# Optimization experiments

Measured on AMD Instinct MI355X. Metric: run time of the kernel, lower is better.

Reference implementation:

```python
import jax, jax.numpy as jnp
import numpy as np

B, N, NC = 16, 25200, 80          # batch, raw predictions, classes (COCO)
CONF_THRES = 0.25
IOU_THRES = 0.45
MAX_CAND = 1000                    # candidates kept after score top-k (pre-NMS)
CLS_OFFSET = 4096.0                # class-wise box offset (non-agnostic NMS trick)
EPS = 1e-7


def setup_inputs() -> dict:
    key = jax.random.key(0)
    # raw head output: [x, y, w, h, obj, cls0..cls79], values in [0,1]
    pred = jax.random.uniform(key, (B, N, 5 + NC), dtype=jnp.float32)
    return {"pred": pred}


def _xywh2xyxy(x):
    xy, wh = x[..., :2], x[..., 2:4]
    return jnp.concatenate([xy - wh * 0.5, xy + wh * 0.5], axis=-1)


def _box_iou(boxes):
    # boxes: [C, 4] xyxy -> pairwise IoU [C, C]
    area = (boxes[:, 2] - boxes[:, 0]) * (boxes[:, 3] - boxes[:, 1])
    lt = jnp.maximum(boxes[:, None, :2], boxes[None, :, :2])
    rb = jnp.minimum(boxes[:, None, 2:], boxes[None, :, 2:])
    wh = jnp.clip(rb - lt, 0.0)
    inter = wh[..., 0] * wh[..., 1]
    return inter / (area[:, None] + area[None, :] - inter + EPS)


def _nms_single(p):
    # p: [N, 5+NC] -> (out [MAX_CAND, 6] xyxy/conf/cls zero-padded, keep [MAX_CAND] bool)
    obj = p[:, 4]
    cls_scores = p[:, 5:] * obj[:, None]          # conf = obj * cls
    conf = jnp.max(cls_scores, axis=-1)
    cls_idx = jnp.argmax(cls_scores, axis=-1)
    valid = (obj > CONF_THRES) & (conf > CONF_THRES)
    score = jnp.where(valid, conf, -1.0)

    # pre-NMS top-k by score (sorted descending) — fixed-shape stand-in for boolean filter
    top_scores, idx = jax.lax.top_k(score, MAX_CAND)
    boxes = _xywh2xyxy(p[idx, :4])                # [C, 4]
    kconf = conf[idx]
    kcls = cls_idx[idx].astype(jnp.float32)
    valid_c = top_scores > 0.0

    # class-offset boxes so different classes never overlap (agnostic=False)
    off_boxes = boxes + kcls[:, None] * CLS_OFFSET
    iou = _box_iou(off_boxes)                     # [C, C]

    ar = jnp.arange(MAX_CAND)

    def body(i, keep):
        sup = keep[i] & (iou[i] > IOU_THRES) & (ar > i)
        return keep & jnp.logical_not(sup)

    keep = jax.lax.fori_loop(0, MAX_CAND, body, valid_c)

    out = jnp.concatenate([boxes, kconf[:, None], kcls[:, None]], axis=-1)  # [C, 6]
    out = jnp.where(keep[:, None], out, 0.0)
    return out, keep


def reference(pred):
    out, keep = jax.vmap(_nms_single)(pred)
    return out, keep
```

## Files before the change

kernel.cpp:

```cpp
#include <hip/hip_runtime.h>
#include <stdint.h>

typedef unsigned int u32;
typedef unsigned long long u64;

#define BATCH 16
#define NANCH 25200
#define NCLS 80
#define ROWF 85
#define MAXC 1000
#define CONF_T 0.25f
#define IOU_T 0.45f
#define EPS_F 1e-7f
#define TILE 64
#define NTILES ((NANCH + TILE - 1) / TILE)

__device__ __forceinline__ float iou_ref(float4 a, float4 b) {
#pragma clang fp contract(off)
  float ai = (a.z - a.x) * (a.w - a.y);
  float aj = (b.z - b.x) * (b.w - b.y);
  float ltx = fmaxf(a.x, b.x), lty = fmaxf(a.y, b.y);
  float rbx = fminf(a.z, b.z), rby = fminf(a.w, b.w);
  float wx = fmaxf(rbx - ltx, 0.0f), wy = fmaxf(rby - lty, 0.0f);
  float inter = wx * wy;
  return inter / (ai + aj - inter + EPS_F);
}

__global__ __launch_bounds__(256) void k1_score(const float* __restrict__ pred,
                                                u64* __restrict__ keys,
                                                u32* __restrict__ hist) {
  __shared__ float srow[TILE * ROWF];
  __shared__ u64 skeys[TILE];
  __shared__ u32 lh[256];
  int tid = threadIdx.x;
  int b = blockIdx.y;
  int t0 = blockIdx.x * TILE;
  int ntile = (t0 + TILE <= NANCH) ? TILE : (NANCH - t0);
  int nf4 = (ntile * ROWF) >> 2;

  lh[tid] = 0;
  const float4* src4 = (const float4*)(pred + ((size_t)b * NANCH + t0) * ROWF);
  float4* smem4 = (float4*)srow;
#pragma unroll
  for (int k = 0; k < 6; ++k) {
    int i = k * 256 + tid;
    if (i < nf4) smem4[i] = src4[i];
  }
  __syncthreads();

  int a = tid >> 2;
  int q = tid & 3;
  float best = -1e30f;
  int bidx = 0;
  float obj = 0.0f;
  if (a < ntile) {
    const float* row = srow + a * ROWF;
    obj = row[4];
    int c0 = q * 20;
#pragma unroll
    for (int c = 0; c < 20; ++c) {
      float s = row[5 + c0 + c] * obj;
      if (s > best) { best = s; bidx = c0 + c; }
    }
  }
#pragma unroll
  for (int off = 1; off < 4; off <<= 1) {
    float ob = __shfl_xor(best, off);
    int oi = __shfl_xor(bidx, off);
    if (ob > best || (ob == best && oi < bidx)) { best = ob; bidx = oi; }
  }
  if (q == 0 && a < ntile) {
    int n = t0 + a;
    bool valid = (obj > CONF_T) && (best > CONF_T);
    u32 hi;
    if (valid) hi = __float_as_uint(best) | 0x80000000u;
    else hi = ((u32)n * 2654435761u) >> 1;
    u32 lo = ((u32)(32767 - n) << 7) | (u32)bidx;
    skeys[a] = ((u64)hi << 32) | lo;
    atomicAdd(&lh[hi >> 24], 1u);
  }
  __syncthreads();
  if (tid < ntile) keys[(size_t)b * NANCH + t0 + tid] = skeys[tid];
  u32 v = lh[tid];
  if (v) atomicAdd(&hist[b * 256 + tid], v);
}

__global__ __launch_bounds__(1024) void k2_select(const float* __restrict__ pred,
                                                  const u64* __restrict__ keys,
                                                  const u32* __restrict__ hist,
                                                  float* __restrict__ selbox,
                                                  float* __restrict__ offbox,
                                                  float* __restrict__ selconf,
                                                  float* __restrict__ selcls,
                                                  u32* __restrict__ selvalid) {
  int b = blockIdx.x;
  int tid = threadIdx.x;
  __shared__ u32 h[256];
  __shared__ u32 sh_sel;
  __shared__ int sh_rank;
  __shared__ u32 scount;
  __shared__ u64 skey[2048];

  const u32* hik = (const u32*)(keys + (size_t)b * NANCH);
  u32 prefix = 0;
  for (int r = 0; r < 4; ++r) {
    if (r == 0) {
      if (tid < 256) h[tid] = hist[b * 256 + tid];
    } else {
      if (tid < 256) h[tid] = 0;
      __syncthreads();
      int shift = 24 - 8 * r;
      for (int i = tid; i < NANCH; i += 1024) {
        u32 hi = hik[2 * i + 1];
        if ((hi >> (shift + 8)) == prefix)
          atomicAdd(&h[(hi >> shift) & 255u], 1u);
      }
    }
    __syncthreads();
    if (tid < 64) {
      int l = tid;
      u32 a0 = h[4 * l + 0], a1 = h[4 * l + 1], a2 = h[4 * l + 2], a3 = h[4 * l + 3];
      u32 lane_sum = a0 + a1 + a2 + a3;
      u32 suf = lane_sum;
#pragma unroll
      for (int off = 1; off < 64; off <<= 1) {
        u32 tv = __shfl_down(suf, off);
        if (l + off < 64) suf += tv;
      }
      int rank = (r == 0) ? MAXC : sh_rank;
      u32 e3 = suf - lane_sum; u32 i3 = e3 + a3;
      u32 e2 = i3;             u32 i2 = e2 + a2;
      u32 e1 = i2;             u32 i1 = e1 + a1;
      u32 e0 = i1;             u32 i0 = e0 + a0;
      if ((int)i3 >= rank && (int)e3 < rank) { sh_sel = 4u * l + 3u; sh_rank = rank - (int)e3; }
      if ((int)i2 >= rank && (int)e2 < rank) { sh_sel = 4u * l + 2u; sh_rank = rank - (int)e2; }
      if ((int)i1 >= rank && (int)e1 < rank) { sh_sel = 4u * l + 1u; sh_rank = rank - (int)e1; }
      if ((int)i0 >= rank && (int)e0 < rank) { sh_sel = 4u * l + 0u; sh_rank = rank - (int)e0; }
    }
    __syncthreads();
    prefix = (r == 0) ? sh_sel : ((prefix << 8) | sh_sel);
  }
  u32 Cstar = prefix;

  if (tid == 0) scount = 0;
  skey[tid] = ~0ull;
  skey[tid + 1024] = ~0ull;
  __syncthreads();
  for (int i = tid; i < NANCH; i += 1024) {
    u64 k = keys[(size_t)b * NANCH + i];
    if ((u32)(k >> 32) >= Cstar) {
      u32 p = atomicAdd(&scount, 1u);
      if (p < 2048) skey[p] = ~k;
    }
  }
  __syncthreads();
  for (u32 kk = 2; kk <= 2048; kk <<= 1) {
    for (u32 j = kk >> 1; j > 0; j >>= 1) {
      for (int idx = tid; idx < 2048; idx += 1024) {
        u32 ixj = (u32)idx ^ j;
        if (ixj > (u32)idx) {
          u64 a = skey[idx], c2 = skey[ixj];
          bool up = ((idx & kk) == 0);
          if (up ? (a > c2) : (a < c2)) { skey[idx] = c2; skey[ixj] = a; }
        }
      }
      __syncthreads();
    }
  }
  if (tid < MAXC) {
    u64 k = ~skey[tid];
    u32 hi = (u32)(k >> 32);
    u32 lo = (u32)k;
    u32 n = 32767u - (lo >> 7);
    u32 ci = lo & 127u;
    bool valid = hi > 0x80000000u;
    float conf = valid ? __uint_as_float(hi & 0x7FFFFFFFu) : 0.0f;
    const float* pr = pred + ((size_t)b * NANCH + n) * ROWF;
    float x = pr[0], y = pr[1], w = pr[2], h2 = pr[3];
    float x1 = x - w * 0.5f, y1 = y - h2 * 0.5f;
    float x2 = x + w * 0.5f, y2 = y + h2 * 0.5f;
    float cf = (float)ci;
    float off = cf * 4096.0f;
    int o4 = (b * MAXC + tid) * 4;
    selbox[o4 + 0] = x1; selbox[o4 + 1] = y1; selbox[o4 + 2] = x2; selbox[o4 + 3] = y2;
    offbox[o4 + 0] = x1 + off; offbox[o4 + 1] = y1 + off;
    offbox[o4 + 2] = x2 + off; offbox[o4 + 3] = y2 + off;
    selconf[b * MAXC + tid] = conf;
    selcls[b * MAXC + tid] = cf;
    selvalid[b * MAXC + tid] = valid ? 1u : 0u;
  }
}

__global__ __launch_bounds__(256) void k3_dt(const float4* __restrict__ offbox4,
                                             u64* __restrict__ dt) {
  int wid = blockIdx.x * 4 + (threadIdx.x >> 6);
  int lane = threadIdx.x & 63;
  int b = wid / MAXC;
  int i = wid % MAXC;
  float4 bi = offbox4[b * MAXC + i];
  u64 myword = 0;
  for (int w = 0; w < 16; ++w) {
    int j = w * 64 + lane;
    int jc = (j < MAXC) ? j : 0;
    float4 bj = offbox4[b * MAXC + jc];
    float iou = iou_ref(bi, bj);
    bool bit = (iou > IOU_T) && (j < i);
    u64 bal = __ballot(bit ? 1 : 0);
    if (lane == w) myword = bal;
  }
  if (lane < 16) dt[((size_t)b * MAXC + i) * 16 + lane] = myword;
}

__global__ __launch_bounds__(1024) void k4_jacobi(const u64* __restrict__ dt,
                                                  const u32* __restrict__ selvalid,
                                                  const float* __restrict__ selbox,
                                                  const float* __restrict__ selconf,
                                                  const float* __restrict__ selcls,
                                                  float* __restrict__ out) {
  int b = blockIdx.x;
  int tid = threadIdx.x;
  int wv = tid >> 6, lane = tid & 63;
  __shared__ u64 keepv[16];
  __shared__ u32 changed;
  bool valid = false;
  u64 dtr[16];
  if (tid < MAXC) {
    valid = selvalid[b * MAXC + tid] != 0u;
#pragma unroll
    for (int w = 0; w < 16; ++w) dtr[w] = dt[((size_t)b * MAXC + tid) * 16 + w];
  } else {
#pragma unroll
    for (int w = 0; w < 16; ++w) dtr[w] = 0ull;
  }
  u64 bal0 = __ballot(valid ? 1 : 0);
  if (tid == 0) changed = 0;
  if (lane == 0) keepv[wv] = bal0;
  __syncthreads();
  for (int pass = 0; pass < MAXC; ++pass) {
    u64 kv[16];
#pragma unroll
    for (int w = 0; w < 16; ++w) kv[w] = keepv[w];
    u64 s = 0;
#pragma unroll
    for (int w = 0; w < 16; ++w) s |= dtr[w] & kv[w];
    bool nk = valid && (s == 0ull);
    u64 bal = __ballot(nk ? 1 : 0);
    __syncthreads();
    if (lane == 0 && bal != kv[wv]) { keepv[wv] = bal; atomicOr(&changed, 1u); }
    __syncthreads();
    u32 ch = changed;
    __syncthreads();
    if (tid == 0) changed = 0;
    if (!ch) break;
  }
  if (tid < MAXC) {
    bool kept = ((keepv[wv] >> lane) & 1ull) != 0ull;
    size_t o = (size_t)b * MAXC + tid;
    const float4* sb4 = (const float4*)selbox;
    float4 bx = sb4[o];
    float cf = selconf[o], cl = selcls[o];
    float* orow = out + o * 6;
    orow[0] = kept ? bx.x : 0.0f;
    orow[1] = kept ? bx.y : 0.0f;
    orow[2] = kept ? bx.z : 0.0f;
    orow[3] = kept ? bx.w : 0.0f;
    orow[4] = kept ? cf : 0.0f;
    orow[5] = kept ? cl : 0.0f;
    out[(size_t)BATCH * MAXC * 6 + o] = kept ? 1.0f : 0.0f;
  }
}

extern "C" void kernel_launch(void* const* d_in, const int* in_sizes, int n_in,
                              void* d_out, int out_size, void* d_ws, size_t ws_size,
                              hipStream_t stream) {
  const float* pred = (const float*)d_in[0];
  float* out = (float*)d_out;
  char* ws = (char*)d_ws;
  size_t off = 0;
  auto alloc = [&](size_t bytes) -> void* {
    void* p = ws + off;
    off = (off + bytes + 255) & ~(size_t)255;
    return p;
  };
  u64* keys     = (u64*)alloc((size_t)BATCH * NANCH * 8);
  u32* hist     = (u32*)alloc((size_t)BATCH * 256 * 4);
  float* selbox = (float*)alloc((size_t)BATCH * MAXC * 4 * 4);
  float* offbox = (float*)alloc((size_t)BATCH * MAXC * 4 * 4);
  float* selconf= (float*)alloc((size_t)BATCH * MAXC * 4);
  float* selcls = (float*)alloc((size_t)BATCH * MAXC * 4);
  u32* selvalid = (u32*)alloc((size_t)BATCH * MAXC * 4);
  u64* dt       = (u64*)alloc((size_t)BATCH * MAXC * 16 * 8);
  (void)ws_size; (void)in_sizes; (void)n_in; (void)out_size;

  hipMemsetAsync(hist, 0, (size_t)BATCH * 256 * 4, stream);

  dim3 g1(NTILES, BATCH);
  k1_score<<<g1, 256, 0, stream>>>(pred, keys, hist);
  k2_select<<<BATCH, 1024, 0, stream>>>(pred, keys, hist, selbox, offbox,
                                        selconf, selcls, selvalid);
  k3_dt<<<(BATCH * MAXC) / 4, 256, 0, stream>>>((const float4*)offbox, dt);
  k4_jacobi<<<BATCH, 1024, 0, stream>>>(dt, selvalid, selbox, selconf,
                                        selcls, out);
}
```

Before: 284.2 us.

## Use 12-bit radix passes, unrolled key scans, float4 stores, transposed suppression matrix

The k2 radix select now runs two 12-bit histogram passes with a 4096-bin shared histogram and a block-wide scan, replacing three 8-bit passes over the keys. Its key scans are unrolled four-way so more global loads are in flight at once. Selected boxes are written with float4 stores. The suppression bitmask is stored word-major so that k4's per-thread loads coalesce. This cuts passes over the 25200 keys per image but adds more shared memory and a larger scan.

Measured after the change: 275.5 us. 1.03x faster.

```diff
diff --git a/kernel.cpp b/kernel.cpp
--- a/kernel.cpp
+++ b/kernel.cpp
@@ -95,50 +95,85 @@
                                                   u32* __restrict__ selvalid) {
   int b = blockIdx.x;
   int tid = threadIdx.x;
-  __shared__ u32 h[256];
+  int wv = tid >> 6, lane = tid & 63;
+  __shared__ u32 h4[4096];
+  __shared__ u32 wsum[16];
   __shared__ u32 sh_sel;
   __shared__ int sh_rank;
   __shared__ u32 scount;
   __shared__ u64 skey[2048];
 
-  const u32* hik = (const u32*)(keys + (size_t)b * NANCH);
-  u32 prefix = 0;
-  for (int r = 0; r < 4; ++r) {
-    if (r == 0) {
-      if (tid < 256) h[tid] = hist[b * 256 + tid];
-    } else {
-      if (tid < 256) h[tid] = 0;
-      __syncthreads();
-      int shift = 24 - 8 * r;
-      for (int i = tid; i < NANCH; i += 1024) {
-        u32 hi = hik[2 * i + 1];
-        if ((hi >> (shift + 8)) == prefix)
-          atomicAdd(&h[(hi >> shift) & 255u], 1u);
-      }
-    }
-    __syncthreads();
-    if (tid < 64) {
-      int l = tid;
-      u32 a0 = h[4 * l + 0], a1 = h[4 * l + 1], a2 = h[4 * l + 2], a3 = h[4 * l + 3];
-      u32 lane_sum = a0 + a1 + a2 + a3;
-      u32 suf = lane_sum;
-#pragma unroll
-      for (int off = 1; off < 64; off <<= 1) {
-        u32 tv = __shfl_down(suf, off);
-        if (l + off < 64) suf += tv;
-      }
-      int rank = (r == 0) ? MAXC : sh_rank;
-      u32 e3 = suf - lane_sum; u32 i3 = e3 + a3;
-      u32 e2 = i3;             u32 i2 = e2 + a2;
-      u32 e1 = i2;             u32 i1 = e1 + a1;
-      u32 e0 = i1;             u32 i0 = e0 + a0;
-      if ((int)i3 >= rank && (int)e3 < rank) { sh_sel = 4u * l + 3u; sh_rank = rank - (int)e3; }
-      if ((int)i2 >= rank && (int)e2 < rank) { sh_sel = 4u * l + 2u; sh_rank = rank - (int)e2; }
-      if ((int)i1 >= rank && (int)e1 < rank) { sh_sel = 4u * l + 1u; sh_rank = rank - (int)e1; }
-      if ((int)i0 >= rank && (int)e0 < rank) { sh_sel = 4u * l + 0u; sh_rank = rank - (int)e0; }
-    }
-    __syncthreads();
-    prefix = (r == 0) ? sh_sel : ((prefix << 8) | sh_sel);
+  const u64* kb = keys + (size_t)b * NANCH;
+
+  if (tid < 256) h4[tid] = hist[b * 256 + tid];
+  __syncthreads();
+  if (tid < 64) {
+    int l = tid;
+    u32 a0 = h4[4 * l], a1 = h4[4 * l + 1], a2 = h4[4 * l + 2], a3 = h4[4 * l + 3];
+    u32 lsum = a0 + a1 + a2 + a3;
+    u32 suf = lsum;
+#pragma unroll
+    for (int off = 1; off < 64; off <<= 1) {
+      u32 tv = __shfl_down(suf, off);
+      if (l + off < 64) suf += tv;
+    }
+    int rank = MAXC;
+    u32 e3 = suf - lsum; u32 i3 = e3 + a3;
+    u32 e2 = i3;         u32 i2 = e2 + a2;
+    u32 e1 = i2;         u32 i1 = e1 + a1;
+    u32 e0 = i1;         u32 i0 = e0 + a0;
+    if ((int)i3 >= rank && (int)e3 < rank) { sh_sel = 4u*l+3u; sh_rank = rank-(int)e3; }
+    if ((int)i2 >= rank && (int)e2 < rank) { sh_sel = 4u*l+2u; sh_rank = rank-(int)e2; }
+    if ((int)i1 >= rank && (int)e1 < rank) { sh_sel = 4u*l+1u; sh_rank = rank-(int)e1; }
+    if ((int)i0 >= rank && (int)e0 < rank) { sh_sel = 4u*l+0u; sh_rank = rank-(int)e0; }
+  }
+  __syncthreads();
+  u32 prefix = sh_sel;
+
+#pragma unroll
+  for (int r = 0; r < 2; ++r) {
+    for (int i = tid; i < 4096; i += 1024) h4[i] = 0;
+    __syncthreads();
+    int psh = (r == 0) ? 24 : 12;
+    int bsh = (r == 0) ? 12 : 0;
+    for (int i0 = tid; i0 < NANCH; i0 += 4096) {
+      int j1 = i0 + 1024, j2 = i0 + 2048, j3 = i0 + 3072;
+      u64 k0 = kb[i0];
+      u64 k1v = (j1 < NANCH) ? kb[j1] : 0;
+      u64 k2v = (j2 < NANCH) ? kb[j2] : 0;
+      u64 k3v = (j3 < NANCH) ? kb[j3] : 0;
+      u32 h0 = (u32)(k0 >> 32), h1 = (u32)(k1v >> 32);
+      u32 h2 = (u32)(k2v >> 32), h3 = (u32)(k3v >> 32);
+      if ((h0 >> psh) == prefix) atomicAdd(&h4[(h0 >> bsh) & 0xFFFu], 1u);
+      if (j1 < NANCH && (h1 >> psh) == prefix) atomicAdd(&h4[(h1 >> bsh) & 0xFFFu], 1u);
+      if (j2 < NANCH && (h2 >> psh) == prefix) atomicAdd(&h4[(h2 >> bsh) & 0xFFFu], 1u);
+      if (j3 < NANCH && (h3 >> psh) == prefix) atomicAdd(&h4[(h3 >> bsh) & 0xFFFu], 1u);
+    }
+    __syncthreads();
+    u32 a0 = h4[4 * tid], a1 = h4[4 * tid + 1], a2 = h4[4 * tid + 2], a3 = h4[4 * tid + 3];
+    u32 lsum = a0 + a1 + a2 + a3;
+    u32 suf = lsum;
+#pragma unroll
+    for (int off = 1; off < 64; off <<= 1) {
+      u32 tv = __shfl_down(suf, off);
+      if (lane + off < 64) suf += tv;
+    }
+    if (lane == 0) wsum[wv] = suf;
+    int rank = sh_rank;
+    __syncthreads();
+    u32 base = 0;
+#pragma unroll
+    for (int w2 = 0; w2 < 16; ++w2) if (w2 > wv) base += wsum[w2];
+    u32 e3 = base + suf - lsum; u32 i3 = e3 + a3;
+    u32 e2 = i3;                u32 i2 = e2 + a2;
+    u32 e1 = i2;                u32 i1 = e1 + a1;
+    u32 e0 = i1;                u32 i0 = e0 + a0;
+    if ((int)i3 >= rank && (int)e3 < rank) { sh_sel = 4u*tid+3u; sh_rank = rank-(int)e3; }
+    if ((int)i2 >= rank && (int)e2 < rank) { sh_sel = 4u*tid+2u; sh_rank = rank-(int)e2; }
+    if ((int)i1 >= rank && (int)e1 < rank) { sh_sel = 4u*tid+1u; sh_rank = rank-(int)e1; }
+    if ((int)i0 >= rank && (int)e0 < rank) { sh_sel = 4u*tid+0u; sh_rank = rank-(int)e0; }
+    __syncthreads();
+    prefix = (prefix << 12) | sh_sel;
   }
   u32 Cstar = prefix;
 
@@ -146,12 +181,16 @@
   skey[tid] = ~0ull;
   skey[tid + 1024] = ~0ull;
   __syncthreads();
-  for (int i = tid; i < NANCH; i += 1024) {
-    u64 k = keys[(size_t)b * NANCH + i];
-    if ((u32)(k >> 32) >= Cstar) {
-      u32 p = atomicAdd(&scount, 1u);
-      if (p < 2048) skey[p] = ~k;
-    }
+  for (int i0 = tid; i0 < NANCH; i0 += 4096) {
+    int j1 = i0 + 1024, j2 = i0 + 2048, j3 = i0 + 3072;
+    u64 k0 = kb[i0];
+    u64 k1v = (j1 < NANCH) ? kb[j1] : 0;
+    u64 k2v = (j2 < NANCH) ? kb[j2] : 0;
+    u64 k3v = (j3 < NANCH) ? kb[j3] : 0;
+    if ((u32)(k0 >> 32) >= Cstar) { u32 p = atomicAdd(&scount, 1u); if (p < 2048) skey[p] = ~k0; }
+    if (j1 < NANCH && (u32)(k1v >> 32) >= Cstar) { u32 p = atomicAdd(&scount, 1u); if (p < 2048) skey[p] = ~k1v; }
+    if (j2 < NANCH && (u32)(k2v >> 32) >= Cstar) { u32 p = atomicAdd(&scount, 1u); if (p < 2048) skey[p] = ~k2v; }
+    if (j3 < NANCH && (u32)(k3v >> 32) >= Cstar) { u32 p = atomicAdd(&scount, 1u); if (p < 2048) skey[p] = ~k3v; }
   }
   __syncthreads();
   for (u32 kk = 2; kk <= 2048; kk <<= 1) {
@@ -181,13 +220,12 @@
     float x2 = x + w * 0.5f, y2 = y + h2 * 0.5f;
     float cf = (float)ci;
     float off = cf * 4096.0f;
-    int o4 = (b * MAXC + tid) * 4;
-    selbox[o4 + 0] = x1; selbox[o4 + 1] = y1; selbox[o4 + 2] = x2; selbox[o4 + 3] = y2;
-    offbox[o4 + 0] = x1 + off; offbox[o4 + 1] = y1 + off;
-    offbox[o4 + 2] = x2 + off; offbox[o4 + 3] = y2 + off;
-    selconf[b * MAXC + tid] = conf;
-    selcls[b * MAXC + tid] = cf;
-    selvalid[b * MAXC + tid] = valid ? 1u : 0u;
+    int o = b * MAXC + tid;
+    ((float4*)selbox)[o] = make_float4(x1, y1, x2, y2);
+    ((float4*)offbox)[o] = make_float4(x1 + off, y1 + off, x2 + off, y2 + off);
+    selconf[o] = conf;
+    selcls[o] = cf;
+    selvalid[o] = valid ? 1u : 0u;
   }
 }
 
@@ -208,7 +246,7 @@
     u64 bal = __ballot(bit ? 1 : 0);
     if (lane == w) myword = bal;
   }
-  if (lane < 16) dt[((size_t)b * MAXC + i) * 16 + lane] = myword;
+  if (lane < 16) dt[((size_t)b * 16 + lane) * MAXC + i] = myword;
 }
 
 __global__ __launch_bounds__(1024) void k4_jacobi(const u64* __restrict__ dt,
@@ -227,7 +265,7 @@
   if (tid < MAXC) {
     valid = selvalid[b * MAXC + tid] != 0u;
 #pragma unroll
-    for (int w = 0; w < 16; ++w) dtr[w] = dt[((size_t)b * MAXC + tid) * 16 + w];
+    for (int w = 0; w < 16; ++w) dtr[w] = dt[((size_t)b * 16 + w) * MAXC + tid];
   } else {
 #pragma unroll
     for (int w = 0; w < 16; ++w) dtr[w] = 0ull;
@@ -289,7 +327,7 @@
   float* selconf= (float*)alloc((size_t)BATCH * MAXC * 4);
   float* selcls = (float*)alloc((size_t)BATCH * MAXC * 4);
   u32* selvalid = (u32*)alloc((size_t)BATCH * MAXC * 4);
-  u64* dt       = (u64*)alloc((size_t)BATCH * MAXC * 16 * 8);
+  u64* dt       = (u64*)alloc(((size_t)BATCH * 16 * MAXC + 1024) * 8);
   (void)ws_size; (void)in_sizes; (void)n_in; (void)out_size;
 
   hipMemsetAsync(hist, 0, (size_t)BATCH * 256 * 4, stream);
```

## Replace 4-pass radix select with 32-bit keys and single 8192-bin histogram

Applied to the files above, without the earlier changes.

Keys shrink from 64-bit to 32-bit by encoding conf minus 0.25 as a float-bit offset plus the class index, with invalid entries set to zero. The select kernel holds all keys in registers, builds one 8192-bin shared histogram and finds the cutoff bin with a block suffix scan, removing the three extra global histogram passes, the global hist buffer and the memset. It also shortens the bitonic sort to 1024 when the candidate count allows, transposes the dt layout so k4 loads are coalesced, and merges conf, class and valid into a single float2 array. Invalid candidates now carry zero boxes instead of real boxes, and tie handling relies on the anchor index packed into the low bits.

Result: faster. 244.5 us (-14.0%).

```diff
diff --git a/kernel.cpp b/kernel.cpp
--- a/kernel.cpp
+++ b/kernel.cpp
@@ -27,18 +27,15 @@
 }
 
 __global__ __launch_bounds__(256) void k1_score(const float* __restrict__ pred,
-                                                u64* __restrict__ keys,
-                                                u32* __restrict__ hist) {
+                                                u32* __restrict__ keys32) {
   __shared__ float srow[TILE * ROWF];
-  __shared__ u64 skeys[TILE];
-  __shared__ u32 lh[256];
+  __shared__ u32 skeys[TILE];
   int tid = threadIdx.x;
   int b = blockIdx.y;
   int t0 = blockIdx.x * TILE;
   int ntile = (t0 + TILE <= NANCH) ? TILE : (NANCH - t0);
   int nf4 = (ntile * ROWF) >> 2;
 
-  lh[tid] = 0;
   const float4* src4 = (const float4*)(pred + ((size_t)b * NANCH + t0) * ROWF);
   float4* smem4 = (float4*)srow;
 #pragma unroll
@@ -70,98 +67,91 @@
     if (ob > best || (ob == best && oi < bidx)) { best = ob; bidx = oi; }
   }
   if (q == 0 && a < ntile) {
-    int n = t0 + a;
     bool valid = (obj > CONF_T) && (best > CONF_T);
-    u32 hi;
-    if (valid) hi = __float_as_uint(best) | 0x80000000u;
-    else hi = ((u32)n * 2654435761u) >> 1;
-    u32 lo = ((u32)(32767 - n) << 7) | (u32)bidx;
-    skeys[a] = ((u64)hi << 32) | lo;
-    atomicAdd(&lh[hi >> 24], 1u);
-  }
-  __syncthreads();
-  if (tid < ntile) keys[(size_t)b * NANCH + t0 + tid] = skeys[tid];
-  u32 v = lh[tid];
-  if (v) atomicAdd(&hist[b * 256 + tid], v);
+    u32 k = valid ? (((__float_as_uint(best) - 0x3E800000u) << 7) | (u32)bidx)
+                  : 0u;
+    skeys[a] = k;
+  }
+  __syncthreads();
+  if (tid < ntile) keys32[(size_t)b * NANCH + t0 + tid] = skeys[tid];
 }
 
 __global__ __launch_bounds__(1024) void k2_select(const float* __restrict__ pred,
-                                                  const u64* __restrict__ keys,
-                                                  const u32* __restrict__ hist,
+                                                  const u32* __restrict__ keys32,
                                                   float* __restrict__ selbox,
                                                   float* __restrict__ offbox,
-                                                  float* __restrict__ selconf,
-                                                  float* __restrict__ selcls,
-                                                  u32* __restrict__ selvalid) {
+                                                  float2* __restrict__ selmeta) {
   int b = blockIdx.x;
   int tid = threadIdx.x;
-  __shared__ u32 h[256];
-  __shared__ u32 sh_sel;
-  __shared__ int sh_rank;
+  int wv = tid >> 6, lane = tid & 63;
+  __shared__ u32 h[8192];
+  __shared__ u64 skey[2048];
+  __shared__ u32 wsum[16];
+  __shared__ u32 sh_fbin;
   __shared__ u32 scount;
-  __shared__ u64 skey[2048];
-
-  const u32* hik = (const u32*)(keys + (size_t)b * NANCH);
-  u32 prefix = 0;
-  for (int r = 0; r < 4; ++r) {
-    if (r == 0) {
-      if (tid < 256) h[tid] = hist[b * 256 + tid];
-    } else {
-      if (tid < 256) h[tid] = 0;
-      __syncthreads();
-      int shift = 24 - 8 * r;
-      for (int i = tid; i < NANCH; i += 1024) {
-        u32 hi = hik[2 * i + 1];
-        if ((hi >> (shift + 8)) == prefix)
-          atomicAdd(&h[(hi >> shift) & 255u], 1u);
-      }
-    }
-    __syncthreads();
-    if (tid < 64) {
-      int l = tid;
-      u32 a0 = h[4 * l + 0], a1 = h[4 * l + 1], a2 = h[4 * l + 2], a3 = h[4 * l + 3];
-      u32 lane_sum = a0 + a1 + a2 + a3;
-      u32 suf = lane_sum;
-#pragma unroll
-      for (int off = 1; off < 64; off <<= 1) {
-        u32 tv = __shfl_down(suf, off);
-        if (l + off < 64) suf += tv;
-      }
-      int rank = (r == 0) ? MAXC : sh_rank;
-      u32 e3 = suf - lane_sum; u32 i3 = e3 + a3;
-      u32 e2 = i3;             u32 i2 = e2 + a2;
-      u32 e1 = i2;             u32 i1 = e1 + a1;
-      u32 e0 = i1;             u32 i0 = e0 + a0;
-      if ((int)i3 >= rank && (int)e3 < rank) { sh_sel = 4u * l + 3u; sh_rank = rank - (int)e3; }
-      if ((int)i2 >= rank && (int)e2 < rank) { sh_sel = 4u * l + 2u; sh_rank = rank - (int)e2; }
-      if ((int)i1 >= rank && (int)e1 < rank) { sh_sel = 4u * l + 1u; sh_rank = rank - (int)e1; }
-      if ((int)i0 >= rank && (int)e0 < rank) { sh_sel = 4u * l + 0u; sh_rank = rank - (int)e0; }
-    }
-    __syncthreads();
-    prefix = (r == 0) ? sh_sel : ((prefix << 8) | sh_sel);
-  }
-  u32 Cstar = prefix;
-
-  if (tid == 0) scount = 0;
+
+  const u32* kb = keys32 + (size_t)b * NANCH;
+  u32 kreg[25];
+#pragma unroll
+  for (int j = 0; j < 25; ++j) {
+    int i = tid + j * 1024;
+    kreg[j] = (i < NANCH) ? kb[i] : 0u;
+  }
+  for (int i = tid; i < 8192; i += 1024) h[i] = 0;
+  if (tid == 0) { sh_fbin = 0; scount = 0; }
   skey[tid] = ~0ull;
   skey[tid + 1024] = ~0ull;
   __syncthreads();
-  for (int i = tid; i < NANCH; i += 1024) {
-    u64 k = keys[(size_t)b * NANCH + i];
-    if ((u32)(k >> 32) >= Cstar) {
+#pragma unroll
+  for (int j = 0; j < 25; ++j) {
+    u32 k = kreg[j];
+    if (k >= 0x80u) atomicAdd(&h[k >> 18], 1u);
+  }
+  __syncthreads();
+  u32 a[8]; u32 lsum = 0;
+#pragma unroll
+  for (int k = 0; k < 8; ++k) { a[k] = h[8 * tid + k]; lsum += a[k]; }
+  u32 suf = lsum;
+#pragma unroll
+  for (int off = 1; off < 64; off <<= 1) {
+    u32 tv = __shfl_down(suf, off);
+    if (lane + off < 64) suf += tv;
+  }
+  if (lane == 0) wsum[wv] = suf;
+  __syncthreads();
+  u32 base = 0;
+#pragma unroll
+  for (int w2 = 0; w2 < 16; ++w2) if (w2 > wv) base += wsum[w2];
+  u32 e = base + suf - lsum;
+#pragma unroll
+  for (int k = 7; k >= 0; --k) {
+    u32 inc = e + a[k];
+    if ((int)inc >= MAXC && (int)e < MAXC) sh_fbin = (u32)(8 * tid + k);
+    e = inc;
+  }
+  __syncthreads();
+  u32 cut = sh_fbin << 18;
+#pragma unroll
+  for (int j = 0; j < 25; ++j) {
+    u32 k = kreg[j];
+    if (k >= cut && k != 0u) {
+      int i = tid + j * 1024;
+      u64 sk = ((u64)(k >> 7) << 32) |
+               (u64)(((32767u - (u32)i) << 7) | (k & 127u));
       u32 p = atomicAdd(&scount, 1u);
-      if (p < 2048) skey[p] = ~k;
-    }
-  }
-  __syncthreads();
-  for (u32 kk = 2; kk <= 2048; kk <<= 1) {
+      if (p < 2048) skey[p] = ~sk;
+    }
+  }
+  __syncthreads();
+  int n = (scount <= 1024u) ? 1024 : 2048;
+  for (u32 kk = 2; kk <= (u32)n; kk <<= 1) {
     for (u32 j = kk >> 1; j > 0; j >>= 1) {
-      for (int idx = tid; idx < 2048; idx += 1024) {
+      for (int idx = tid; idx < n; idx += 1024) {
         u32 ixj = (u32)idx ^ j;
         if (ixj > (u32)idx) {
-          u64 a = skey[idx], c2 = skey[ixj];
+          u64 x = skey[idx], y = skey[ixj];
           bool up = ((idx & kk) == 0);
-          if (up ? (a > c2) : (a < c2)) { skey[idx] = c2; skey[ixj] = a; }
+          if (up ? (x > y) : (x < y)) { skey[idx] = y; skey[ixj] = x; }
         }
       }
       __syncthreads();
@@ -169,25 +159,25 @@
   }
   if (tid < MAXC) {
     u64 k = ~skey[tid];
-    u32 hi = (u32)(k >> 32);
+    u32 confpart = (u32)(k >> 32);
     u32 lo = (u32)k;
-    u32 n = 32767u - (lo >> 7);
-    u32 ci = lo & 127u;
-    bool valid = hi > 0x80000000u;
-    float conf = valid ? __uint_as_float(hi & 0x7FFFFFFFu) : 0.0f;
-    const float* pr = pred + ((size_t)b * NANCH + n) * ROWF;
-    float x = pr[0], y = pr[1], w = pr[2], h2 = pr[3];
-    float x1 = x - w * 0.5f, y1 = y - h2 * 0.5f;
-    float x2 = x + w * 0.5f, y2 = y + h2 * 0.5f;
-    float cf = (float)ci;
-    float off = cf * 4096.0f;
-    int o4 = (b * MAXC + tid) * 4;
-    selbox[o4 + 0] = x1; selbox[o4 + 1] = y1; selbox[o4 + 2] = x2; selbox[o4 + 3] = y2;
-    offbox[o4 + 0] = x1 + off; offbox[o4 + 1] = y1 + off;
-    offbox[o4 + 2] = x2 + off; offbox[o4 + 3] = y2 + off;
-    selconf[b * MAXC + tid] = conf;
-    selcls[b * MAXC + tid] = cf;
-    selvalid[b * MAXC + tid] = valid ? 1u : 0u;
+    bool valid = confpart != 0u;
+    float conf = 0.0f, x1 = 0.0f, y1 = 0.0f, x2 = 0.0f, y2 = 0.0f;
+    float cf = 0.0f, offv = 0.0f;
+    if (valid) {
+      u32 nidx = 32767u - ((lo >> 7) & 0x7FFFu);
+      u32 ci = lo & 127u;
+      conf = __uint_as_float(confpart + 0x3E800000u);
+      const float* pr = pred + ((size_t)b * NANCH + nidx) * ROWF;
+      float x = pr[0], y = pr[1], w = pr[2], h2 = pr[3];
+      x1 = x - w * 0.5f; y1 = y - h2 * 0.5f;
+      x2 = x + w * 0.5f; y2 = y + h2 * 0.5f;
+      cf = (float)ci; offv = cf * 4096.0f;
+    }
+    int o = b * MAXC + tid;
+    ((float4*)selbox)[o] = make_float4(x1, y1, x2, y2);
+    ((float4*)offbox)[o] = make_float4(x1 + offv, y1 + offv, x2 + offv, y2 + offv);
+    selmeta[o] = make_float2(conf, cf);
   }
 }
 
@@ -208,14 +198,12 @@
     u64 bal = __ballot(bit ? 1 : 0);
     if (lane == w) myword = bal;
   }
-  if (lane < 16) dt[((size_t)b * MAXC + i) * 16 + lane] = myword;
+  if (lane < 16) dt[((size_t)b * 16 + lane) * MAXC + i] = myword;
 }
 
 __global__ __launch_bounds__(1024) void k4_jacobi(const u64* __restrict__ dt,
-                                                  const u32* __restrict__ selvalid,
+                                                  const float2* __restrict__ selmeta,
                                                   const float* __restrict__ selbox,
-                                                  const float* __restrict__ selconf,
-                                                  const float* __restrict__ selcls,
                                                   float* __restrict__ out) {
   int b = blockIdx.x;
   int tid = threadIdx.x;
@@ -223,11 +211,13 @@
   __shared__ u64 keepv[16];
   __shared__ u32 changed;
   bool valid = false;
+  float2 meta = make_float2(0.0f, 0.0f);
   u64 dtr[16];
   if (tid < MAXC) {
-    valid = selvalid[b * MAXC + tid] != 0u;
-#pragma unroll
-    for (int w = 0; w < 16; ++w) dtr[w] = dt[((size_t)b * MAXC + tid) * 16 + w];
+    meta = selmeta[b * MAXC + tid];
+    valid = meta.x > 0.0f;
+#pragma unroll
+    for (int w = 0; w < 16; ++w) dtr[w] = dt[((size_t)b * 16 + w) * MAXC + tid];
   } else {
 #pragma unroll
     for (int w = 0; w < 16; ++w) dtr[w] = 0ull;
@@ -256,16 +246,14 @@
   if (tid < MAXC) {
     bool kept = ((keepv[wv] >> lane) & 1ull) != 0ull;
     size_t o = (size_t)b * MAXC + tid;
-    const float4* sb4 = (const float4*)selbox;
-    float4 bx = sb4[o];
-    float cf = selconf[o], cl = selcls[o];
+    float4 bx = ((const float4*)selbox)[o];
     float* orow = out + o * 6;
     orow[0] = kept ? bx.x : 0.0f;
     orow[1] = kept ? bx.y : 0.0f;
     orow[2] = kept ? bx.z : 0.0f;
     orow[3] = kept ? bx.w : 0.0f;
-    orow[4] = kept ? cf : 0.0f;
-    orow[5] = kept ? cl : 0.0f;
+    orow[4] = kept ? meta.x : 0.0f;
+    orow[5] = kept ? meta.y : 0.0f;
     out[(size_t)BATCH * MAXC * 6 + o] = kept ? 1.0f : 0.0f;
   }
 }
@@ -282,23 +270,16 @@
     off = (off + bytes + 255) & ~(size_t)255;
     return p;
   };
-  u64* keys     = (u64*)alloc((size_t)BATCH * NANCH * 8);
-  u32* hist     = (u32*)alloc((size_t)BATCH * 256 * 4);
+  u32* keys32   = (u32*)alloc((size_t)BATCH * NANCH * 4);
   float* selbox = (float*)alloc((size_t)BATCH * MAXC * 4 * 4);
   float* offbox = (float*)alloc((size_t)BATCH * MAXC * 4 * 4);
-  float* selconf= (float*)alloc((size_t)BATCH * MAXC * 4);
-  float* selcls = (float*)alloc((size_t)BATCH * MAXC * 4);
-  u32* selvalid = (u32*)alloc((size_t)BATCH * MAXC * 4);
-  u64* dt       = (u64*)alloc((size_t)BATCH * MAXC * 16 * 8);
+  float2* selmeta = (float2*)alloc((size_t)BATCH * MAXC * 8);
+  u64* dt       = (u64*)alloc((size_t)BATCH * 16 * MAXC * 8);
   (void)ws_size; (void)in_sizes; (void)n_in; (void)out_size;
 
-  hipMemsetAsync(hist, 0, (size_t)BATCH * 256 * 4, stream);
-
   dim3 g1(NTILES, BATCH);
-  k1_score<<<g1, 256, 0, stream>>>(pred, keys, hist);
-  k2_select<<<BATCH, 1024, 0, stream>>>(pred, keys, hist, selbox, offbox,
-                                        selconf, selcls, selvalid);
+  k1_score<<<g1, 256, 0, stream>>>(pred, keys32);
+  k2_select<<<BATCH, 1024, 0, stream>>>(pred, keys32, selbox, offbox, selmeta);
   k3_dt<<<(BATCH * MAXC) / 4, 256, 0, stream>>>((const float4*)offbox, dt);
-  k4_jacobi<<<BATCH, 1024, 0, stream>>>(dt, selvalid, selbox, selconf,
-                                        selcls, out);
-}
+  k4_jacobi<<<BATCH, 1024, 0, stream>>>(dt, selmeta, selbox, out);
+}
```
